# Performance work log

Measured on AMD Instinct MI355X. Metric: run time of the kernel, lower is better.

The kernel has to match this reference:

```python
import jax, jax.numpy as jnp
import numpy as np

B, S, D_MODEL, D_QK, D_VO = 4, 2048, 1024, 128, 128
NEG = -1.0e9


def setup_inputs() -> dict:
    key = jax.random.key(0)
    k1, k2, k3, k4, k5 = jax.random.split(key, 5)
    enc = jax.random.normal(k1, (B, S, D_MODEL), dtype=jnp.float32)
    # causal mask: True means masked (masked_fill), broadcast over batch
    causal = jnp.triu(jnp.ones((S, S), dtype=bool), k=1)
    mask = jnp.broadcast_to(causal, (B, S, S))
    scale = 0.02
    W_q = jax.random.normal(k2, (D_MODEL, D_QK), dtype=jnp.float32) * scale
    W_k = jax.random.normal(k3, (D_MODEL, D_QK), dtype=jnp.float32) * scale
    W_v = jax.random.normal(k4, (D_MODEL, D_VO), dtype=jnp.float32) * scale
    W_o = jax.random.normal(k5, (D_VO, D_MODEL), dtype=jnp.float32) * scale
    return {"encodings": enc, "mask": mask, "W_q": W_q, "W_k": W_k, "W_v": W_v, "W_o": W_o}


def reference(encodings, mask, W_q, W_k, W_v, W_o):
    # q,k: [B,S,d_qk]; v: [B,S,d_vo]
    q = jnp.einsum('bsd,de->bse', encodings, W_q)
    k = jnp.einsum('bsd,de->bse', encodings, W_k)
    v = jnp.einsum('bsd,de->bse', encodings, W_v)
    sims = jnp.einsum('bqe,bke->bqk', q, k) / jnp.asarray(D_QK ** 0.5, q.dtype)
    sims = jnp.where(mask, jnp.asarray(NEG, sims.dtype), sims)
    attn = jax.nn.softmax(sims, axis=-1)  # [B,S,S]
    scores = jnp.einsum('bqk,bke->bqe', attn, v)  # [B,S,d_vo]
    return jnp.einsum('bse,ed->bsd', scores, W_o)  # [B,S,d_model]
```

## Files before the change

### kernel.cpp

```cpp
#include <hip/hip_runtime.h>
#include <hip/hip_bf16.h>
#include <stdint.h>

typedef __attribute__((ext_vector_type(8))) short short8;
typedef __attribute__((ext_vector_type(4))) float floatx4;

using bf16 = __hip_bfloat16;

#define LOG2E 1.4426950408889634f
#define SCALE_L2 0.12751793359133147f

__device__ inline unsigned short f2b(float f) {
    bf16 h = __float2bfloat16(f);
    return *(unsigned short*)&h;
}

__global__ __launch_bounds__(256) void prep_all(const float4* __restrict__ enc4,
                                                ushort4* __restrict__ encb4,
                                                const float* __restrict__ Wq,
                                                const float* __restrict__ Wk,
                                                const float* __restrict__ Wv,
                                                const float* __restrict__ Wo,
                                                bf16* __restrict__ Wqkvt,
                                                bf16* __restrict__ Wot) {
    int bx = blockIdx.x;
    if (bx < 8192) {
        int i = bx * 256 + threadIdx.x;
        float4 v = enc4[i];
        ushort4 o;
        o.x = f2b(v.x); o.y = f2b(v.y); o.z = f2b(v.z); o.w = f2b(v.w);
        encb4[i] = o;
    } else {
        int idx = (bx - 8192) * 256 + threadIdx.x;
        int sel = idx >> 17;
        int i = idx & 131071;
        if (sel < 3) {
            const float* W = (sel == 0) ? Wq : (sel == 1) ? Wk : Wv;
            int r = i >> 7, c = i & 127;
            Wqkvt[(size_t)(sel * 128 + c) * 1024 + r] = __float2bfloat16(W[i]);
        } else {
            int r = i >> 10, c = i & 1023;
            Wot[(size_t)c * 128 + r] = __float2bfloat16(Wo[i]);
        }
    }
}

template <int KDIM, bool QKV>
__global__ __launch_bounds__(256) void gemm64(const bf16* __restrict__ A, int lda,
                                              const bf16* __restrict__ Bt, int ldb,
                                              void* __restrict__ C0,
                                              void* __restrict__ C1,
                                              void* __restrict__ C2) {
    __shared__ bf16 As[64 * 40];
    __shared__ bf16 Bs[128 * 40];

    const int tid = threadIdx.x;
    const int m0 = blockIdx.x * 64;
    const int nsel = blockIdx.y;
    const int brow0 = nsel * 128;
    const int w = tid >> 6, lane = tid & 63;
    const int wm = (w >> 1) * 32, wn = (w & 1) * 64;
    const int quad = lane >> 4, l16 = lane & 15;

    const int ra = tid >> 2, ca = (tid & 3) * 8;
    const int rb0 = tid >> 2, rb1 = (tid + 256) >> 2;

    floatx4 acc[2][4];
#pragma unroll
    for (int i = 0; i < 2; i++)
#pragma unroll
        for (int j = 0; j < 4; j++) acc[i][j] = (floatx4){0.f, 0.f, 0.f, 0.f};

    int4 pa, pb0, pb1;
    pa  = *(const int4*)&A[(size_t)(m0 + ra) * lda + ca];
    pb0 = *(const int4*)&Bt[(size_t)(brow0 + rb0) * ldb + ca];
    pb1 = *(const int4*)&Bt[(size_t)(brow0 + rb1) * ldb + ca];

    for (int k0 = 0; k0 < KDIM; k0 += 32) {
        __syncthreads();
        *(int4*)&As[ra * 40 + ca] = pa;
        *(int4*)&Bs[rb0 * 40 + ca] = pb0;
        *(int4*)&Bs[rb1 * 40 + ca] = pb1;
        __syncthreads();

        if (k0 + 32 < KDIM) {
            pa  = *(const int4*)&A[(size_t)(m0 + ra) * lda + k0 + 32 + ca];
            pb0 = *(const int4*)&Bt[(size_t)(brow0 + rb0) * ldb + k0 + 32 + ca];
            pb1 = *(const int4*)&Bt[(size_t)(brow0 + rb1) * ldb + k0 + 32 + ca];
        }

        short8 a[2], b[4];
#pragma unroll
        for (int mt = 0; mt < 2; mt++)
            a[mt] = *(const short8*)&As[(wm + mt * 16 + l16) * 40 + quad * 8];
#pragma unroll
        for (int nt = 0; nt < 4; nt++)
            b[nt] = *(const short8*)&Bs[(wn + nt * 16 + l16) * 40 + quad * 8];
#pragma unroll
        for (int mt = 0; mt < 2; mt++)
#pragma unroll
            for (int nt = 0; nt < 4; nt++)
                acc[mt][nt] = __builtin_amdgcn_mfma_f32_16x16x32_bf16(a[mt], b[nt], acc[mt][nt], 0, 0, 0);
    }

#pragma unroll
    for (int mt = 0; mt < 2; mt++)
#pragma unroll
        for (int nt = 0; nt < 4; nt++)
#pragma unroll
            for (int r = 0; r < 4; r++) {
                int row = m0 + wm + mt * 16 + quad * 4 + r;
                int col = wn + nt * 16 + l16;
                float v = acc[mt][nt][r];
                if (QKV) {
                    bf16 h = __float2bfloat16(v);
                    if (nsel == 0) {
                        ((bf16*)C0)[(size_t)row * 128 + col] = h;
                    } else if (nsel == 1) {
                        ((bf16*)C1)[(size_t)row * 128 + col] = h;
                    } else {
                        int bb = row >> 11, ss = row & 2047;
                        ((bf16*)C2)[(size_t)bb * 262144 + (size_t)col * 2048 + ss] = h;
                    }
                } else {
                    ((float*)C0)[(size_t)row * 1024 + brow0 + col] = v;
                }
            }
}

__global__ __launch_bounds__(256) void flash_split(const bf16* __restrict__ Q,
                                                   const bf16* __restrict__ K,
                                                   const bf16* __restrict__ Vt,
                                                   float* __restrict__ Op,
                                                   float2* __restrict__ Ml) {
    __shared__ bf16 Ks[64 * 136];
    __shared__ bf16 Vs[128 * 72];
    __shared__ bf16 Ps[4 * 16 * 72];

    const int tid = threadIdx.x;
    const int b = blockIdx.x >> 5;
    const int qt = blockIdx.x & 31;
    const int ks = blockIdx.y;
    const int q0 = qt * 64;
    const int w = tid >> 6, lane = tid & 63;
    const int quad = lane >> 4, l16 = lane & 15;

    const int ntiles = qt + 1;
    const int per = (ntiles + 3) >> 2;
    const int start = ks * per;
    const int end = min(start + per, ntiles);

    const int qrow = q0 + w * 16 + l16;
    short8 qf[4];
#pragma unroll
    for (int k4 = 0; k4 < 4; k4++)
        qf[k4] = *(const short8*)&Q[((size_t)b * 2048 + qrow) * 128 + k4 * 32 + quad * 8];

    float m_run = -1.0e30f, l_run = 0.f;
    floatx4 o[8];
#pragma unroll
    for (int d = 0; d < 8; d++) o[d] = (floatx4){0.f, 0.f, 0.f, 0.f};

    int4 kreg[4], vreg[4];
    const int sr[4]  = {(tid + 0) >> 4, (tid + 256) >> 4, (tid + 512) >> 4, (tid + 768) >> 4};
    const int scg    = (tid & 15) * 8;
    const int sr2[4] = {(tid + 0) >> 3, (tid + 256) >> 3, (tid + 512) >> 3, (tid + 768) >> 3};
    const int scg2   = (tid & 7) * 8;

    if (start < end) {
#pragma unroll
        for (int i = 0; i < 4; i++) {
            kreg[i] = *(const int4*)&K[((size_t)b * 2048 + start * 64 + sr[i]) * 128 + scg];
            vreg[i] = *(const int4*)&Vt[(size_t)b * 262144 + (size_t)sr2[i] * 2048 + start * 64 + scg2];
        }
    }

    for (int kt = start; kt < end; kt++) {
        __syncthreads();
#pragma unroll
        for (int i = 0; i < 4; i++) {
            *(int4*)&Ks[sr[i] * 136 + scg] = kreg[i];
            *(int4*)&Vs[sr2[i] * 72 + scg2] = vreg[i];
        }
        __syncthreads();

        if (kt + 1 < end) {
#pragma unroll
            for (int i = 0; i < 4; i++) {
                kreg[i] = *(const int4*)&K[((size_t)b * 2048 + (kt + 1) * 64 + sr[i]) * 128 + scg];
                vreg[i] = *(const int4*)&Vt[(size_t)b * 262144 + (size_t)sr2[i] * 2048 + (kt + 1) * 64 + scg2];
            }
        }

        floatx4 s_acc[4];
#pragma unroll
        for (int nt = 0; nt < 4; nt++) {
            s_acc[nt] = (floatx4){0.f, 0.f, 0.f, 0.f};
#pragma unroll
            for (int k4 = 0; k4 < 4; k4++) {
                short8 kf = *(const short8*)&Ks[(nt * 16 + l16) * 136 + k4 * 32 + quad * 8];
                s_acc[nt] = __builtin_amdgcn_mfma_f32_16x16x32_bf16(kf, qf[k4], s_acc[nt], 0, 0, 0);
            }
        }

        float sv[4][4];
#pragma unroll
        for (int nt = 0; nt < 4; nt++)
#pragma unroll
            for (int r = 0; r < 4; r++) {
                float s = s_acc[nt][r] * SCALE_L2;
                if (kt == qt) {
                    int kcol = kt * 64 + nt * 16 + quad * 4 + r;
                    if (kcol > qrow) s = -1.0e9f;
                }
                sv[nt][r] = s;
            }

        float t0 = fmaxf(fmaxf(sv[0][0], sv[0][1]), fmaxf(sv[0][2], sv[0][3]));
        float t1 = fmaxf(fmaxf(sv[1][0], sv[1][1]), fmaxf(sv[1][2], sv[1][3]));
        float t2 = fmaxf(fmaxf(sv[2][0], sv[2][1]), fmaxf(sv[2][2], sv[2][3]));
        float t3 = fmaxf(fmaxf(sv[3][0], sv[3][1]), fmaxf(sv[3][2], sv[3][3]));
        float tmax = fmaxf(fmaxf(t0, t1), fmaxf(t2, t3));
        tmax = fmaxf(tmax, __shfl_xor(tmax, 16));
        tmax = fmaxf(tmax, __shfl_xor(tmax, 32));

        float mnew = fmaxf(m_run, tmax);
        float alpha = exp2f(m_run - mnew);
        m_run = mnew;

        float rsum = 0.f;
#pragma unroll
        for (int nt = 0; nt < 4; nt++)
#pragma unroll
            for (int r = 0; r < 4; r++) {
                float p = exp2f(sv[nt][r] - mnew);
                sv[nt][r] = p;
                rsum += p;
            }
        rsum += __shfl_xor(rsum, 16);
        rsum += __shfl_xor(rsum, 32);
        l_run = l_run * alpha + rsum;

#pragma unroll
        for (int nt = 0; nt < 4; nt++) {
            ushort4 pk;
            pk.x = f2b(sv[nt][0]); pk.y = f2b(sv[nt][1]);
            pk.z = f2b(sv[nt][2]); pk.w = f2b(sv[nt][3]);
            *(ushort4*)&Ps[w * 1152 + l16 * 72 + nt * 16 + quad * 4] = pk;
        }

#pragma unroll
        for (int d = 0; d < 8; d++) {
            o[d][0] *= alpha; o[d][1] *= alpha; o[d][2] *= alpha; o[d][3] *= alpha;
        }

        short8 pf[2];
#pragma unroll
        for (int k2 = 0; k2 < 2; k2++)
            pf[k2] = *(const short8*)&Ps[w * 1152 + l16 * 72 + k2 * 32 + quad * 8];
#pragma unroll
        for (int d = 0; d < 8; d++)
#pragma unroll
            for (int k2 = 0; k2 < 2; k2++) {
                short8 vf = *(const short8*)&Vs[(d * 16 + l16) * 72 + k2 * 32 + quad * 8];
                o[d] = __builtin_amdgcn_mfma_f32_16x16x32_bf16(vf, pf[k2], o[d], 0, 0, 0);
            }
    }

    const size_t orow = (size_t)ks * 8192 + b * 2048 + qrow;
#pragma unroll
    for (int d = 0; d < 8; d++) {
        float4 v = {o[d][0], o[d][1], o[d][2], o[d][3]};
        *(float4*)&Op[orow * 128 + d * 16 + quad * 4] = v;
    }
    if (lane < 16) Ml[orow] = make_float2(m_run, l_run);
}

__global__ __launch_bounds__(256) void flash_merge(const float* __restrict__ Op,
                                                   const float2* __restrict__ Ml,
                                                   bf16* __restrict__ Sc) {
    int idx = blockIdx.x * 256 + threadIdx.x;
    int row = idx >> 5, dg = (idx & 31) * 4;

    float2 ml[4];
#pragma unroll
    for (int s = 0; s < 4; s++) ml[s] = Ml[(size_t)s * 8192 + row];
    float M = fmaxf(fmaxf(ml[0].x, ml[1].x), fmaxf(ml[2].x, ml[3].x));
    float L = 0.f, wgt[4];
#pragma unroll
    for (int s = 0; s < 4; s++) {
        wgt[s] = exp2f(ml[s].x - M);
        L += ml[s].y * wgt[s];
    }
    float4 acc = {0.f, 0.f, 0.f, 0.f};
#pragma unroll
    for (int s = 0; s < 4; s++) {
        float4 v = *(const float4*)&Op[((size_t)s * 8192 + row) * 128 + dg];
        acc.x += v.x * wgt[s]; acc.y += v.y * wgt[s];
        acc.z += v.z * wgt[s]; acc.w += v.w * wgt[s];
    }
    float inv = 1.0f / L;
    ushort4 o;
    o.x = f2b(acc.x * inv); o.y = f2b(acc.y * inv);
    o.z = f2b(acc.z * inv); o.w = f2b(acc.w * inv);
    *(ushort4*)&Sc[(size_t)row * 128 + dg] = o;
}

extern "C" void kernel_launch(void* const* d_in, const int* in_sizes, int n_in,
                              void* d_out, int out_size, void* d_ws, size_t ws_size,
                              hipStream_t stream) {
    const float* enc = (const float*)d_in[0];
    const float* Wq = (const float*)d_in[2];
    const float* Wk = (const float*)d_in[3];
    const float* Wv = (const float*)d_in[4];
    const float* Wo = (const float*)d_in[5];
    float* out = (float*)d_out;

    const size_t MB = 1024 * 1024;
    char* ws = (char*)d_ws;
    bf16*   encb  = (bf16*)(ws);
    float*  Op    = (float*)(ws);
    bf16*   Qb    = (bf16*)(ws + 16 * MB);
    bf16*   Kb    = (bf16*)(ws + 18 * MB);
    bf16*   Vtb   = (bf16*)(ws + 20 * MB);
    bf16*   Scb   = (bf16*)(ws + 22 * MB);
    bf16*   Wqkvt = (bf16*)(ws + 24 * MB);
    bf16*   Wot   = (bf16*)(ws + 24 * MB + 768 * 1024);
    float2* Ml    = (float2*)(ws + 25 * MB);

    prep_all<<<10240, 256, 0, stream>>>((const float4*)enc, (ushort4*)encb,
                                        Wq, Wk, Wv, Wo, Wqkvt, Wot);

    dim3 blk(256);
    gemm64<1024, true><<<dim3(128, 3), blk, 0, stream>>>(encb, 1024, Wqkvt, 1024,
                                                         Qb, Kb, Vtb);

    flash_split<<<dim3(128, 4), blk, 0, stream>>>(Qb, Kb, Vtb, Op, Ml);
    flash_merge<<<1024, blk, 0, stream>>>(Op, Ml, Scb);

    gemm64<128, false><<<dim3(128, 8), blk, 0, stream>>>(Scb, 128, Wot, 128,
                                                         out, nullptr, nullptr);
}
```

Before: 215.4 us.

## Read K/V fragments directly from global memory and split QKV GEMM into smaller tiles

The flash attention kernel no longer stages K and V tiles through shared memory with register prefetch and barriers. Each wave now loads its MFMA fragments straight from global memory and relies on the L1/L2 caches for reuse across the four waves. The QKV projection GEMM is also changed to 64x64 output tiles with twice as many blocks, which raises occupancy and parallelism. The trade-off is that each block reads K/V from global memory four times, the loads are not software-prefetched, and the V-transpose reads are strided.

```diff
diff --git a/kernel.cpp b/kernel.cpp
--- a/kernel.cpp
+++ b/kernel.cpp
@@ -7,7 +7,6 @@
 
 using bf16 = __hip_bfloat16;
 
-#define LOG2E 1.4426950408889634f
 #define SCALE_L2 0.12751793359133147f
 
 __device__ inline unsigned short f2b(float f) {
@@ -45,19 +44,88 @@
     }
 }
 
-template <int KDIM, bool QKV>
-__global__ __launch_bounds__(256) void gemm64(const bf16* __restrict__ A, int lda,
-                                              const bf16* __restrict__ Bt, int ldb,
-                                              void* __restrict__ C0,
-                                              void* __restrict__ C1,
-                                              void* __restrict__ C2) {
+__global__ __launch_bounds__(256) void gemm_qkv64(const bf16* __restrict__ A,
+                                                  const bf16* __restrict__ Bt,
+                                                  bf16* __restrict__ Qb,
+                                                  bf16* __restrict__ Kb,
+                                                  bf16* __restrict__ Vtb) {
+    __shared__ bf16 As[64 * 40];
+    __shared__ bf16 Bs[64 * 40];
+
+    const int tid = threadIdx.x;
+    const int m0 = blockIdx.x * 64;
+    const int brow0 = blockIdx.y * 64;
+    const int proj = brow0 >> 7;
+    const int colb = brow0 & 127;
+    const int w = tid >> 6, lane = tid & 63;
+    const int wm = (w >> 1) * 32, wn = (w & 1) * 32;
+    const int quad = lane >> 4, l16 = lane & 15;
+
+    const int ra = tid >> 2, ca = (tid & 3) * 8;
+
+    floatx4 acc[2][2];
+#pragma unroll
+    for (int i = 0; i < 2; i++)
+#pragma unroll
+        for (int j = 0; j < 2; j++) acc[i][j] = (floatx4){0.f, 0.f, 0.f, 0.f};
+
+    int4 pa = *(const int4*)&A[(size_t)(m0 + ra) * 1024 + ca];
+    int4 pb = *(const int4*)&Bt[(size_t)(brow0 + ra) * 1024 + ca];
+
+    for (int k0 = 0; k0 < 1024; k0 += 32) {
+        __syncthreads();
+        *(int4*)&As[ra * 40 + ca] = pa;
+        *(int4*)&Bs[ra * 40 + ca] = pb;
+        __syncthreads();
+
+        if (k0 + 32 < 1024) {
+            pa = *(const int4*)&A[(size_t)(m0 + ra) * 1024 + k0 + 32 + ca];
+            pb = *(const int4*)&Bt[(size_t)(brow0 + ra) * 1024 + k0 + 32 + ca];
+        }
+
+        short8 a[2], b[2];
+#pragma unroll
+        for (int mt = 0; mt < 2; mt++)
+            a[mt] = *(const short8*)&As[(wm + mt * 16 + l16) * 40 + quad * 8];
+#pragma unroll
+        for (int nt = 0; nt < 2; nt++)
+            b[nt] = *(const short8*)&Bs[(wn + nt * 16 + l16) * 40 + quad * 8];
+#pragma unroll
+        for (int mt = 0; mt < 2; mt++)
+#pragma unroll
+            for (int nt = 0; nt < 2; nt++)
+                acc[mt][nt] = __builtin_amdgcn_mfma_f32_16x16x32_bf16(a[mt], b[nt], acc[mt][nt], 0, 0, 0);
+    }
+
+#pragma unroll
+    for (int mt = 0; mt < 2; mt++)
+#pragma unroll
+        for (int nt = 0; nt < 2; nt++)
+#pragma unroll
+            for (int r = 0; r < 4; r++) {
+                int row = m0 + wm + mt * 16 + quad * 4 + r;
+                int col = colb + wn + nt * 16 + l16;
+                bf16 h = __float2bfloat16(acc[mt][nt][r]);
+                if (proj == 0) {
+                    Qb[(size_t)row * 128 + col] = h;
+                } else if (proj == 1) {
+                    Kb[(size_t)row * 128 + col] = h;
+                } else {
+                    int bb = row >> 11, ss = row & 2047;
+                    Vtb[(size_t)bb * 262144 + (size_t)col * 2048 + ss] = h;
+                }
+            }
+}
+
+__global__ __launch_bounds__(256) void gemm_out(const bf16* __restrict__ A,
+                                                const bf16* __restrict__ Bt,
+                                                float* __restrict__ C) {
     __shared__ bf16 As[64 * 40];
     __shared__ bf16 Bs[128 * 40];
 
     const int tid = threadIdx.x;
     const int m0 = blockIdx.x * 64;
-    const int nsel = blockIdx.y;
-    const int brow0 = nsel * 128;
+    const int n0 = blockIdx.y * 128;
     const int w = tid >> 6, lane = tid & 63;
     const int wm = (w >> 1) * 32, wn = (w & 1) * 64;
     const int quad = lane >> 4, l16 = lane & 15;
@@ -71,22 +139,21 @@
 #pragma unroll
         for (int j = 0; j < 4; j++) acc[i][j] = (floatx4){0.f, 0.f, 0.f, 0.f};
 
-    int4 pa, pb0, pb1;
-    pa  = *(const int4*)&A[(size_t)(m0 + ra) * lda + ca];
-    pb0 = *(const int4*)&Bt[(size_t)(brow0 + rb0) * ldb + ca];
-    pb1 = *(const int4*)&Bt[(size_t)(brow0 + rb1) * ldb + ca];
-
-    for (int k0 = 0; k0 < KDIM; k0 += 32) {
+    int4 pa  = *(const int4*)&A[(size_t)(m0 + ra) * 128 + ca];
+    int4 pb0 = *(const int4*)&Bt[(size_t)(n0 + rb0) * 128 + ca];
+    int4 pb1 = *(const int4*)&Bt[(size_t)(n0 + rb1) * 128 + ca];
+
+    for (int k0 = 0; k0 < 128; k0 += 32) {
         __syncthreads();
         *(int4*)&As[ra * 40 + ca] = pa;
         *(int4*)&Bs[rb0 * 40 + ca] = pb0;
         *(int4*)&Bs[rb1 * 40 + ca] = pb1;
         __syncthreads();
 
-        if (k0 + 32 < KDIM) {
-            pa  = *(const int4*)&A[(size_t)(m0 + ra) * lda + k0 + 32 + ca];
-            pb0 = *(const int4*)&Bt[(size_t)(brow0 + rb0) * ldb + k0 + 32 + ca];
-            pb1 = *(const int4*)&Bt[(size_t)(brow0 + rb1) * ldb + k0 + 32 + ca];
+        if (k0 + 32 < 128) {
+            pa  = *(const int4*)&A[(size_t)(m0 + ra) * 128 + k0 + 32 + ca];
+            pb0 = *(const int4*)&Bt[(size_t)(n0 + rb0) * 128 + k0 + 32 + ca];
+            pb1 = *(const int4*)&Bt[(size_t)(n0 + rb1) * 128 + k0 + 32 + ca];
         }
 
         short8 a[2], b[4];
@@ -110,21 +177,8 @@
 #pragma unroll
             for (int r = 0; r < 4; r++) {
                 int row = m0 + wm + mt * 16 + quad * 4 + r;
-                int col = wn + nt * 16 + l16;
-                float v = acc[mt][nt][r];
-                if (QKV) {
-                    bf16 h = __float2bfloat16(v);
-                    if (nsel == 0) {
-                        ((bf16*)C0)[(size_t)row * 128 + col] = h;
-                    } else if (nsel == 1) {
-                        ((bf16*)C1)[(size_t)row * 128 + col] = h;
-                    } else {
-                        int bb = row >> 11, ss = row & 2047;
-                        ((bf16*)C2)[(size_t)bb * 262144 + (size_t)col * 2048 + ss] = h;
-                    }
-                } else {
-                    ((float*)C0)[(size_t)row * 1024 + brow0 + col] = v;
-                }
+                int col = n0 + wn + nt * 16 + l16;
+                C[(size_t)row * 1024 + col] = acc[mt][nt][r];
             }
 }
 
@@ -133,8 +187,6 @@
                                                    const bf16* __restrict__ Vt,
                                                    float* __restrict__ Op,
                                                    float2* __restrict__ Ml) {
-    __shared__ bf16 Ks[64 * 136];
-    __shared__ bf16 Vs[128 * 72];
     __shared__ bf16 Ps[4 * 16 * 72];
 
     const int tid = threadIdx.x;
@@ -151,46 +203,23 @@
     const int end = min(start + per, ntiles);
 
     const int qrow = q0 + w * 16 + l16;
+    const bf16* Qrow = &Q[((size_t)b * 2048 + qrow) * 128];
     short8 qf[4];
 #pragma unroll
     for (int k4 = 0; k4 < 4; k4++)
-        qf[k4] = *(const short8*)&Q[((size_t)b * 2048 + qrow) * 128 + k4 * 32 + quad * 8];
+        qf[k4] = *(const short8*)&Qrow[k4 * 32 + quad * 8];
+
+    const bf16* Kb = &K[(size_t)b * 2048 * 128];
+    const bf16* Vb = &Vt[(size_t)b * 262144];
 
     float m_run = -1.0e30f, l_run = 0.f;
     floatx4 o[8];
 #pragma unroll
     for (int d = 0; d < 8; d++) o[d] = (floatx4){0.f, 0.f, 0.f, 0.f};
 
-    int4 kreg[4], vreg[4];
-    const int sr[4]  = {(tid + 0) >> 4, (tid + 256) >> 4, (tid + 512) >> 4, (tid + 768) >> 4};
-    const int scg    = (tid & 15) * 8;
-    const int sr2[4] = {(tid + 0) >> 3, (tid + 256) >> 3, (tid + 512) >> 3, (tid + 768) >> 3};
-    const int scg2   = (tid & 7) * 8;
-
-    if (start < end) {
-#pragma unroll
-        for (int i = 0; i < 4; i++) {
-            kreg[i] = *(const int4*)&K[((size_t)b * 2048 + start * 64 + sr[i]) * 128 + scg];
-            vreg[i] = *(const int4*)&Vt[(size_t)b * 262144 + (size_t)sr2[i] * 2048 + start * 64 + scg2];
-        }
-    }
-
     for (int kt = start; kt < end; kt++) {
-        __syncthreads();
-#pragma unroll
-        for (int i = 0; i < 4; i++) {
-            *(int4*)&Ks[sr[i] * 136 + scg] = kreg[i];
-            *(int4*)&Vs[sr2[i] * 72 + scg2] = vreg[i];
-        }
-        __syncthreads();
-
-        if (kt + 1 < end) {
-#pragma unroll
-            for (int i = 0; i < 4; i++) {
-                kreg[i] = *(const int4*)&K[((size_t)b * 2048 + (kt + 1) * 64 + sr[i]) * 128 + scg];
-                vreg[i] = *(const int4*)&Vt[(size_t)b * 262144 + (size_t)sr2[i] * 2048 + (kt + 1) * 64 + scg2];
-            }
-        }
+        const bf16* Kt = Kb + (size_t)(kt * 64) * 128;
+        const bf16* Vtt = Vb + kt * 64;
 
         floatx4 s_acc[4];
 #pragma unroll
@@ -198,7 +227,7 @@
             s_acc[nt] = (floatx4){0.f, 0.f, 0.f, 0.f};
 #pragma unroll
             for (int k4 = 0; k4 < 4; k4++) {
-                short8 kf = *(const short8*)&Ks[(nt * 16 + l16) * 136 + k4 * 32 + quad * 8];
+                short8 kf = *(const short8*)&Kt[(size_t)(nt * 16 + l16) * 128 + k4 * 32 + quad * 8];
                 s_acc[nt] = __builtin_amdgcn_mfma_f32_16x16x32_bf16(kf, qf[k4], s_acc[nt], 0, 0, 0);
             }
         }
@@ -262,7 +291,7 @@
         for (int d = 0; d < 8; d++)
 #pragma unroll
             for (int k2 = 0; k2 < 2; k2++) {
-                short8 vf = *(const short8*)&Vs[(d * 16 + l16) * 72 + k2 * 32 + quad * 8];
+                short8 vf = *(const short8*)&Vtt[(size_t)(d * 16 + l16) * 2048 + k2 * 32 + quad * 8];
                 o[d] = __builtin_amdgcn_mfma_f32_16x16x32_bf16(vf, pf[k2], o[d], 0, 0, 0);
             }
     }
@@ -332,12 +361,10 @@
                                         Wq, Wk, Wv, Wo, Wqkvt, Wot);
 
     dim3 blk(256);
-    gemm64<1024, true><<<dim3(128, 3), blk, 0, stream>>>(encb, 1024, Wqkvt, 1024,
-                                                         Qb, Kb, Vtb);
+    gemm_qkv64<<<dim3(128, 6), blk, 0, stream>>>(encb, Wqkvt, Qb, Kb, Vtb);
 
     flash_split<<<dim3(128, 4), blk, 0, stream>>>(Qb, Kb, Vtb, Op, Ml);
     flash_merge<<<1024, blk, 0, stream>>>(Op, Ml, Scb);
 
-    gemm64<128, false><<<dim3(128, 8), blk, 0, stream>>>(Scb, 128, Wot, 128,
-                                                         out, nullptr, nullptr);
-}
+    gemm_out<<<dim3(128, 8), blk, 0, stream>>>(Scb, Wot, out);
+}
```

Result: slower. 222.0 us (+3.0%).
